# Kernel tuning notes

Hardware: AMD Instinct MI355X
Metric: run time of the kernel (lower is better)

The kernel has to match this reference:

```python
import jax, jax.numpy as jnp
import numpy as np

B, N, P, L = 32, 4096, 256, 16
DR = 128           # rel_dim = args.rgcn_hidden_size
H = 128            # rnn_hidden_size (unidirectional -> rnn_opt_dim == H)
D = H
NUM_REL = 400      # num_rels * 2


def setup_inputs() -> dict:
    key = jax.random.key(0)
    ks = jax.random.split(key, 12)
    s = 0.05
    graph_embed = jax.random.normal(ks[0], (B, N, DR), jnp.float32)
    node_opt = jax.random.normal(ks[1], (B, D), jnp.float32)
    node_idx = jax.random.randint(ks[2], (B, P, L), 0, N)
    rel_idx = jax.random.randint(ks[3], (B, P, L), 0, NUM_REL)
    path_lens = jax.random.randint(ks[4], (B, P), 1, L + 1)  # in [1, L]
    rel_embeds = jax.random.normal(ks[5], (NUM_REL, DR), jnp.float32) * s
    W_ih = jax.random.normal(ks[6], (4 * H, 2 * DR), jnp.float32) * s
    W_hh = jax.random.normal(ks[7], (4 * H, H), jnp.float32) * s
    b_ih = jnp.zeros((4 * H,), jnp.float32)
    b_hh = jnp.zeros((4 * H,), jnp.float32)
    in_proj_w = jax.random.normal(ks[8], (3 * D, D), jnp.float32) * s
    in_proj_b = jnp.zeros((3 * D,), jnp.float32)
    out_proj_w = jax.random.normal(ks[9], (D, D), jnp.float32) * s
    out_proj_b = jnp.zeros((D,), jnp.float32)
    return dict(graph_embed=graph_embed, node_opt=node_opt, rel_embeds=rel_embeds,
                W_ih=W_ih, W_hh=W_hh, b_ih=b_ih, b_hh=b_hh,
                in_proj_w=in_proj_w, in_proj_b=in_proj_b,
                out_proj_w=out_proj_w, out_proj_b=out_proj_b,
                node_idx=node_idx, rel_idx=rel_idx, path_lens=path_lens)


def _forward(graph_embed, node_opt, rel_embeds, W_ih, W_hh, b_ih, b_hh,
             in_proj_w, in_proj_b, out_proj_w, out_proj_b,
             node_idx, rel_idx, path_lens):
    b, n, dr = graph_embed.shape
    p, l = node_idx.shape[1], node_idx.shape[2]
    h = W_hh.shape[1]
    dt = graph_embed.dtype

    t = jnp.arange(l)
    # node embedding valid for steps < len; rel valid for steps < len-1 ('Padr' at last step -> zero rel half)
    node_mask = (t[None, None, :] < path_lens[:, :, None]).astype(dt)[..., None]
    rel_mask = (t[None, None, :] < (path_lens - 1)[:, :, None]).astype(dt)[..., None]

    batch_ix = jnp.arange(b)[:, None, None]
    node_e = graph_embed[batch_ix, node_idx]            # [B,P,L,DR]
    rel_e = rel_embeds[rel_idx]                          # [B,P,L,DR]
    x = jnp.concatenate([node_e * node_mask, rel_e * rel_mask], axis=-1)
    x = x.reshape(b * p, l, 2 * dr)                      # packed path sequences

    bias = b_ih + b_hh

    def step(carry, xt):
        hh, cc = carry
        g = xt @ W_ih.T + hh @ W_hh.T + bias
        i, f, gg, o = jnp.split(g, 4, axis=-1)
        i = jax.nn.sigmoid(i); f = jax.nn.sigmoid(f)
        gg = jnp.tanh(gg); o = jax.nn.sigmoid(o)
        cc = f * cc + i * gg
        hh = o * jnp.tanh(cc)
        return (hh, cc), hh

    h0 = jnp.zeros((b * p, h), dt)
    _, ys = jax.lax.scan(step, (h0, h0), jnp.swapaxes(x, 0, 1))
    ys = jnp.swapaxes(ys, 0, 1).reshape(b, p, l, h)

    # last valid LSTM output per path (== pack_padded_sequence semantics, unidirectional)
    idx = jnp.broadcast_to((path_lens - 1)[:, :, None, None], (b, p, 1, h))
    last = jnp.take_along_axis(ys, idx, axis=2).squeeze(2)   # [B,P,H]

    # single-head MultiheadAttention: query = node_opt, keys/values = path encodings
    Wq, Wk, Wv = jnp.split(in_proj_w, 3, axis=0)
    bq, bk, bv = jnp.split(in_proj_b, 3)
    q = node_opt @ Wq.T + bq                                  # [B,D]
    k = last @ Wk.T + bk                                      # [B,P,D]
    v = last @ Wv.T + bv
    scale = 1.0 / jnp.sqrt(jnp.asarray(q.shape[-1], dt))
    attn = jax.nn.softmax(jnp.einsum('bd,bpd->bp', q, k) * scale, axis=-1)
    ctx = jnp.einsum('bp,bpd->bd', attn, v)
    return ctx @ out_proj_w.T + out_proj_b                    # [B,D]


def reference(graph_embed, node_opt, rel_embeds, W_ih, W_hh, b_ih, b_hh,
              in_proj_w, in_proj_b, out_proj_w, out_proj_b,
              node_idx, rel_idx, path_lens):
    return _forward(graph_embed, node_opt, rel_embeds, W_ih, W_hh, b_ih, b_hh,
                    in_proj_w, in_proj_b, out_proj_w, out_proj_b,
                    node_idx, rel_idx, path_lens)
```

## Files before the change

### kernel.cpp

```cpp
#include <hip/hip_runtime.h>
#include <hip/hip_bf16.h>


#define B_    32
#define N_    4096
#define L_    16
#define DR_   128
#define H_    128
#define G4_   512
#define AST2  264
#define NPATH 8192
#define NPB   16

typedef unsigned short bfraw;
typedef short short8 __attribute__((ext_vector_type(8)));
typedef float f32x4 __attribute__((ext_vector_type(4)));

__device__ int   g_isbf16;
__device__ int   g_isi64;
__device__ __align__(16) bfraw g_Wcat[G4_ * 256];
__device__ __align__(16) float g_relproj[400 * G4_];
__device__ float g_bias[G4_];
__device__ int   g_perm[NPATH];
__device__ float g_last[NPATH * H_];

#define BAR() asm volatile("s_waitcnt lgkmcnt(0)\n\ts_barrier" ::: "memory")

__device__ __forceinline__ float bfc(bfraw v) {
    return __uint_as_float(((unsigned)v) << 16);
}
__device__ __forceinline__ bfraw f2b(float f) {
    unsigned u = __float_as_uint(f);
    return (bfraw)((u + 0x7FFFu + ((u >> 16) & 1u)) >> 16);
}
__device__ __forceinline__ unsigned pk2(float a, float b) {
    return (unsigned)f2b(a) | ((unsigned)f2b(b) << 16);
}
__device__ __forceinline__ float ld(const void* p, size_t i, int isbf) {
    return isbf ? bfc(((const bfraw*)p)[i]) : ((const float*)p)[i];
}
__device__ __forceinline__ float sigf(float x) {
    return __builtin_amdgcn_rcpf(1.0f + __expf(-x));
}
__device__ __forceinline__ float tanhfast(float x) {
    return 2.0f * sigf(2.0f * x) - 1.0f;
}

__device__ __forceinline__ float dot128(const float* __restrict__ w,
                                        const float* __restrict__ s) {
    float acc = 0.f;
    #pragma unroll
    for (int i = 0; i < 32; ++i) {
        const float4 wv = *(const float4*)(w + i * 4);
        acc = fmaf(wv.x, s[i*4+0], fmaf(wv.y, s[i*4+1],
              fmaf(wv.z, s[i*4+2], fmaf(wv.w, s[i*4+3], acc))));
    }
    return acc;
}

__global__ __launch_bounds__(512) void k_prep(
    const void* __restrict__ node_opt, const int* __restrict__ node_idx,
    const void* __restrict__ rel_embeds,
    const void* __restrict__ W_ih, const void* __restrict__ W_hh,
    const void* __restrict__ b_ih, const void* __restrict__ b_hh,
    const int* __restrict__ path_lens)
{
    __shared__ float relv[DR_];
    __shared__ int s_big, s_nz, hist[16], cur[16];
    const int tid = threadIdx.x;
    const int blk = blockIdx.x;

    if (tid == 0) { s_big = 0; s_nz = 0; }
    __syncthreads();
    {
        const unsigned short* u = (const unsigned short*)node_opt;
        int big = 0;
        #pragma unroll
        for (int i = 0; i < 4; ++i) {
            const float v = fabsf(bfc(u[tid + i * 512]));
            big |= !(v < 1.0e3f);
        }
        if (big) s_big = 1;
        if (node_idx[2 * tid + 1] != 0) s_nz = 1;
    }
    __syncthreads();
    const int isbf = s_big ? 0 : 1;
    const int i64  = s_nz ? 0 : 1;

    if (blk < 400) {
        const int r = blk;
        if (tid < DR_) relv[tid] = ld(rel_embeds, (size_t)r * DR_ + tid, isbf);
        __syncthreads();
        const int n = tid;
        float s;
        if (isbf) {
            s = 0.f;
            for (int d = 0; d < DR_; ++d)
                s = fmaf(relv[d], bfc(((const bfraw*)W_ih)[(size_t)n * 256 + 128 + d]), s);
        } else {
            s = dot128((const float*)W_ih + (size_t)n * 256 + 128, relv);
        }
        g_relproj[r * G4_ + ((n & 127) << 2) + (n >> 7)] = s;
    } else if (blk < 656) {
        const int idx = (blk - 400) * 512 + tid;
        const int n = idx >> 8, k = idx & 255;
        const float v = (k < H_) ? ld(W_hh, (size_t)n * H_ + k, isbf)
                                 : ld(W_ih, (size_t)n * 256 + (k - H_), isbf);
        g_Wcat[n * 256 + k] = f2b(v);
    } else {
        if (tid == 0) { g_isbf16 = isbf; g_isi64 = i64; }
        g_bias[tid] = ld(b_ih, tid, isbf) + ld(b_hh, tid, isbf);
        if (tid < 16) hist[tid] = 0;
        __syncthreads();
        for (int p = tid; p < NPATH; p += 512) {
            const int len = i64 ? path_lens[2 * p] : path_lens[p];
            atomicAdd(&hist[len - 1], 1);
        }
        __syncthreads();
        if (tid == 0) {
            int off = 0;
            for (int b = 15; b >= 0; --b) { cur[b] = off; off += hist[b]; }
        }
        __syncthreads();
        for (int p = tid; p < NPATH; p += 512) {
            const int len = i64 ? path_lens[2 * p] : path_lens[p];
            const int pos = atomicAdd(&cur[len - 1], 1);
            g_perm[pos] = p;
        }
    }
}

__global__ __launch_bounds__(512, 2) void k_lstm(
    const void* __restrict__ graph_embed,
    const int*  __restrict__ node_idx,
    const int*  __restrict__ rel_idx,
    const int*  __restrict__ path_lens)
{
    __shared__ __align__(16) bfraw Abuf[2][NPB][AST2];
    __shared__ int s_pid[NPB], s_len[NPB];
    __shared__ int s_nid[NPB][L_], s_rid[NPB][L_];

    const int isbf = g_isbf16;
    const int i64  = g_isi64;
    const int tid  = threadIdx.x;

    if (tid < NPB) {
        const int pid = g_perm[blockIdx.x * NPB + tid];
        s_pid[tid] = pid;
        s_len[tid] = i64 ? path_lens[2 * pid] : path_lens[pid];
    }
    __syncthreads();
    if (tid < 256) {
        const int m = tid >> 4, t = tid & 15;
        const int idx = s_pid[m] * L_ + t;
        s_nid[m][t] = i64 ? node_idx[2 * idx] : node_idx[idx];
        s_rid[m][t] = i64 ? rel_idx[2 * idx]  : rel_idx[idx];
    }
    if (tid < 256) {
        const int m = tid >> 4, i0 = (tid & 15) * 8;
        *(uint4*)&Abuf[0][m][i0] = make_uint4(0, 0, 0, 0);
    }
    __syncthreads();

    int maxlen = 0;
    #pragma unroll
    for (int m = 0; m < NPB; ++m) maxlen = max(maxlen, s_len[m]);

    const int w    = tid >> 6;
    const int l    = tid & 63;
    const int quad = l >> 4;
    const int col  = l & 15;
    const int u0   = w * 16 + col;

    short8 wreg[8][4];
    float bq4[4];
    #pragma unroll
    for (int g = 0; g < 4; ++g) {
        bq4[g] = g_bias[g * 128 + u0];
        const bfraw* wrow = g_Wcat + (size_t)(g * 128 + u0) * 256 + quad * 8;
        #pragma unroll
        for (int ck = 0; ck < 8; ++ck)
            wreg[ck][g] = *(const short8*)(wrow + ck * 32);
    }

    const int pm  = tid >> 5;
    const int pi0 = (tid & 31) * 4;
    const size_t gbase = (size_t)(s_pid[pm] >> 8) * (size_t)(N_ * DR_);

    uint4 pnA, pnB;

    {
        const int nid = s_nid[pm][0];
        uint2 npk;
        if (isbf) {
            const uint2 q = *(const uint2*)((const bfraw*)graph_embed + gbase + (size_t)nid * DR_ + pi0);
            npk = q;
        } else {
            const float* gp = (const float*)graph_embed + gbase + (size_t)nid * DR_ + pi0;
            const uint4 q = *(const uint4*)gp;
            const float* a = (const float*)&q;
            npk = make_uint2(pk2(a[0], a[1]), pk2(a[2], a[3]));
        }
        *(uint2*)&Abuf[0][pm][128 + pi0] = npk;
    }
    if (maxlen > 1) {
        const int nid = s_nid[pm][1];
        if (isbf) {
            const uint2 q = *(const uint2*)((const bfraw*)graph_embed + gbase + (size_t)nid * DR_ + pi0);
            pnA.x = q.x; pnA.y = q.y;
        } else {
            pnA = *(const uint4*)((const float*)graph_embed + gbase + (size_t)nid * DR_ + pi0);
        }
    }
    __syncthreads();

    float c[4];
    #pragma unroll
    for (int r = 0; r < 4; ++r) c[r] = 0.f;

    bfraw (*Ar)[AST2] = Abuf[0];
    bfraw (*Aw)[AST2] = Abuf[1];

    for (int t = 0; t < maxlen; ++t) {
        const bool more = (t + 1 < maxlen);

        if (t + 2 < maxlen) {
            const int nid = s_nid[pm][t + 2];
            if (isbf) {
                const uint2 q = *(const uint2*)((const bfraw*)graph_embed + gbase + (size_t)nid * DR_ + pi0);
                pnB.x = q.x; pnB.y = q.y;
            } else {
                pnB = *(const uint4*)((const float*)graph_embed + gbase + (size_t)nid * DR_ + pi0);
            }
        }

        f32x4 acc[4];
        #pragma unroll
        for (int g = 0; g < 4; ++g) {
            const float b = bq4[g];
            acc[g][0] = b; acc[g][1] = b; acc[g][2] = b; acc[g][3] = b;
        }
        #pragma unroll
        for (int ck = 0; ck < 8; ++ck) {
            const short8 a0 = *(const short8*)&Ar[col][ck * 32 + quad * 8];
            #pragma unroll
            for (int g = 0; g < 4; ++g)
                acc[g] = __builtin_amdgcn_mfma_f32_16x16x32_bf16(a0, wreg[ck][g], acc[g], 0, 0, 0);
        }
        __builtin_amdgcn_sched_barrier(0);

        f32x4 rlv[4];
        #pragma unroll
        for (int r = 0; r < 4; ++r) {
            const int m = quad * 4 + r;
            rlv[r] = *(const f32x4*)(g_relproj + (size_t)s_rid[m][t] * G4_ + u0 * 4);
        }

        #pragma unroll
        for (int r = 0; r < 4; ++r) {
            const int m = quad * 4 + r;
            const float relm = (t < s_len[m] - 1) ? 1.0f : 0.0f;
            const float ig = sigf(acc[0][r] + relm * rlv[r][0]);
            const float fg = sigf(acc[1][r] + relm * rlv[r][1]);
            const float gg = tanhfast(acc[2][r] + relm * rlv[r][2]);
            const float og = sigf(acc[3][r] + relm * rlv[r][3]);
            const float cc = fg * c[r] + ig * gg;
            c[r] = cc;
            const float h = og * tanhfast(cc);
            Aw[m][u0] = f2b(h);
            if (t == s_len[m] - 1)
                g_last[(size_t)s_pid[m] * H_ + u0] = h;
        }

        if (more) {
            uint2 npk = make_uint2(0, 0);
            if (t + 1 < s_len[pm]) {
                if (isbf) npk = make_uint2(pnA.x, pnA.y);
                else {
                    const float* a = (const float*)&pnA;
                    npk = make_uint2(pk2(a[0], a[1]), pk2(a[2], a[3]));
                }
            }
            *(uint2*)&Aw[pm][128 + pi0] = npk;
            pnA = pnB;
        }

        BAR();
        bfraw (*tmp)[AST2] = Ar; Ar = Aw; Aw = tmp;
    }
}

__global__ __launch_bounds__(256) void k_attn(
    const void* __restrict__ node_opt,
    const void* __restrict__ in_proj_w,
    const void* __restrict__ in_proj_b,
    const void* __restrict__ out_proj_w,
    const void* __restrict__ out_proj_b,
    float* __restrict__ out)
{
    const int isbf = g_isbf16;
    const int b = blockIdx.x, tid = threadIdx.x;
    __shared__ __align__(16) float s_no[128], q[128], qk[128], sv2[2][128], ctx[128];
    __shared__ float logits[256];
    __shared__ float red[12];

    const int u    = tid & 127;
    const int half = tid >> 7;

    if (tid < 128) s_no[tid] = ld(node_opt, b * 128 + tid, isbf);
    __syncthreads();
    {
        float s = 0.f;
        const int j0 = half * 64;
        if (isbf) {
            #pragma unroll 8
            for (int j = 0; j < 64; ++j)
                s = fmaf(s_no[j0 + j], ld(in_proj_w, (size_t)u * 128 + j0 + j, 1), s);
        } else {
            const float* wr = (const float*)in_proj_w + (size_t)u * 128 + j0;
            #pragma unroll
            for (int i = 0; i < 16; ++i) {
                const float4 wv = *(const float4*)(wr + i * 4);
                s = fmaf(wv.x, s_no[j0+i*4+0], fmaf(wv.y, s_no[j0+i*4+1],
                    fmaf(wv.z, s_no[j0+i*4+2], fmaf(wv.w, s_no[j0+i*4+3], s))));
            }
        }
        sv2[half][u] = s;
    }
    __syncthreads();
    if (tid < 128) q[tid] = sv2[0][tid] + sv2[1][tid] + ld(in_proj_b, tid, isbf);
    __syncthreads();
    {
        float s = 0.f;
        const int j0 = half * 64;
        #pragma unroll 8
        for (int j = 0; j < 64; ++j)
            s = fmaf(q[j0 + j], ld(in_proj_w, (size_t)(128 + j0 + j) * 128 + u, isbf), s);
        sv2[half][u] = s;
    }
    if (tid == 0) {
        float s = 0.f;
        #pragma unroll 8
        for (int j = 0; j < 128; ++j)
            s = fmaf(q[j], ld(in_proj_b, 128 + j, isbf), s);
        red[10] = s;
    }
    __syncthreads();
    if (tid < 128) qk[tid] = sv2[0][tid] + sv2[1][tid];
    __syncthreads();
    {
        const float* lp = g_last + ((size_t)b * 256 + tid) * H_;
        const float s = dot128(lp, qk);
        logits[tid] = (s + red[10]) * 0.08838834764831845f;
    }
    __syncthreads();
    float v = logits[tid];
    #pragma unroll
    for (int off = 32; off > 0; off >>= 1) v = fmaxf(v, __shfl_xor(v, off, 64));
    if ((tid & 63) == 0) red[tid >> 6] = v;
    __syncthreads();
    if (tid == 0) red[8] = fmaxf(fmaxf(red[0], red[1]), fmaxf(red[2], red[3]));
    __syncthreads();
    const float e = __expf(logits[tid] - red[8]);
    float sum = e;
    #pragma unroll
    for (int off = 32; off > 0; off >>= 1) sum += __shfl_xor(sum, off, 64);
    if ((tid & 63) == 0) red[4 + (tid >> 6)] = sum;
    __syncthreads();
    if (tid == 0) red[9] = red[4] + red[5] + red[6] + red[7];
    __syncthreads();
    logits[tid] = e / red[9];
    __syncthreads();
    {
        float s = 0.f;
        const float* lb = g_last + ((size_t)b * 256 + half * 128) * H_ + u;
        #pragma unroll 8
        for (int p = 0; p < 128; ++p)
            s = fmaf(logits[half * 128 + p], lb[(size_t)p * H_], s);
        sv2[half][u] = s;
    }
    __syncthreads();
    if (tid < 128) q[tid] = sv2[0][tid] + sv2[1][tid];
    __syncthreads();
    if (tid < 128) {
        float s;
        if (isbf) {
            s = 0.f;
            #pragma unroll 8
            for (int j = 0; j < 128; ++j)
                s = fmaf(q[j], ld(in_proj_w, (size_t)(256 + tid) * 128 + j, 1), s);
        } else {
            s = dot128((const float*)in_proj_w + (size_t)(256 + tid) * 128, q);
        }
        ctx[tid] = s + ld(in_proj_b, 256 + tid, isbf);
    }
    __syncthreads();
    if (tid < 128) {
        float s;
        if (isbf) {
            s = 0.f;
            #pragma unroll 8
            for (int d = 0; d < 128; ++d)
                s = fmaf(ctx[d], ld(out_proj_w, (size_t)tid * 128 + d, 1), s);
        } else {
            s = dot128((const float*)out_proj_w + (size_t)tid * 128, ctx);
        }
        out[b * 128 + tid] = s + ld(out_proj_b, tid, isbf);
    }
}

extern "C" void kernel_launch(void* const* d_in, const int* in_sizes, int n_in,
                              void* d_out, int out_size, void* d_ws, size_t ws_size,
                              hipStream_t stream)
{
    const void* graph_embed = d_in[0];
    const void* node_opt    = d_in[1];
    const void* rel_embeds  = d_in[2];
    const void* W_ih        = d_in[3];
    const void* W_hh        = d_in[4];
    const void* b_ih        = d_in[5];
    const void* b_hh        = d_in[6];
    const void* in_proj_w   = d_in[7];
    const void* in_proj_b   = d_in[8];
    const void* out_proj_w  = d_in[9];
    const void* out_proj_b  = d_in[10];
    const int* node_idx  = (const int*)d_in[11];
    const int* rel_idx   = (const int*)d_in[12];
    const int* path_lens = (const int*)d_in[13];
    (void)d_ws; (void)ws_size; (void)in_sizes; (void)n_in; (void)out_size;

    hipLaunchKernelGGL(k_prep, dim3(657), dim3(512), 0, stream,
                       node_opt, node_idx, rel_embeds, W_ih, W_hh, b_ih, b_hh,
                       path_lens);
    hipLaunchKernelGGL(k_lstm, dim3(NPATH / NPB), dim3(512), 0, stream,
                       graph_embed, node_idx, rel_idx, path_lens);
    hipLaunchKernelGGL(k_attn, dim3(B_), dim3(256), 0, stream,
                       node_opt, in_proj_w, in_proj_b, out_proj_w, out_proj_b,
                       (float*)d_out);
}
```

Before: 205.4 us.

## Double paths per block and stage recurrent weights in LDS instead of registers

```diff
diff --git a/kernel.cpp b/kernel.cpp
--- a/kernel.cpp
+++ b/kernel.cpp
@@ -10,7 +10,7 @@
 #define G4_   512
 #define AST2  264
 #define NPATH 8192
-#define NPB   16
+#define NPB   32
 
 typedef unsigned short bfraw;
 typedef short short8 __attribute__((ext_vector_type(8)));
@@ -130,13 +130,14 @@
     }
 }
 
-__global__ __launch_bounds__(512, 2) void k_lstm(
+__global__ __launch_bounds__(1024, 4) void k_lstm(
     const void* __restrict__ graph_embed,
     const int*  __restrict__ node_idx,
     const int*  __restrict__ rel_idx,
     const int*  __restrict__ path_lens)
 {
-    __shared__ __align__(16) bfraw Abuf[2][NPB][AST2];
+    __shared__ __align__(16) bfraw Whh[4][4][G4_][8];
+    __shared__ __align__(16) bfraw A[NPB][AST2];
     __shared__ int s_pid[NPB], s_len[NPB];
     __shared__ int s_nid[NPB][L_], s_rid[NPB][L_];
 
@@ -150,15 +151,20 @@
         s_len[tid] = i64 ? path_lens[2 * pid] : path_lens[pid];
     }
     __syncthreads();
-    if (tid < 256) {
+    if (tid < 512) {
         const int m = tid >> 4, t = tid & 15;
         const int idx = s_pid[m] * L_ + t;
         s_nid[m][t] = i64 ? node_idx[2 * idx] : node_idx[idx];
         s_rid[m][t] = i64 ? rel_idx[2 * idx]  : rel_idx[idx];
     }
-    if (tid < 256) {
+    if (tid < 512) {
         const int m = tid >> 4, i0 = (tid & 15) * 8;
-        *(uint4*)&Abuf[0][m][i0] = make_uint4(0, 0, 0, 0);
+        *(uint4*)&A[m][i0] = make_uint4(0, 0, 0, 0);
+    }
+    for (int i = tid; i < 4 * 4 * G4_; i += 1024) {
+        const int n = i & 511, q = (i >> 9) & 3, ck = i >> 11;
+        *(uint4*)&Whh[ck][q][n][0] =
+            *(const uint4*)(g_Wcat + (size_t)n * 256 + ck * 32 + q * 8);
     }
     __syncthreads();
 
@@ -166,22 +172,18 @@
     #pragma unroll
     for (int m = 0; m < NPB; ++m) maxlen = max(maxlen, s_len[m]);
 
-    const int w    = tid >> 6;
+    const int wid  = tid >> 6;
+    const int tile = wid >> 3;
+    const int w8   = wid & 7;
     const int l    = tid & 63;
     const int quad = l >> 4;
     const int col  = l & 15;
-    const int u0   = w * 16 + col;
-
-    short8 wreg[8][4];
+    const int u0   = w8 * 16 + col;
+    const int mrow = tile * 16;
+
     float bq4[4];
     #pragma unroll
-    for (int g = 0; g < 4; ++g) {
-        bq4[g] = g_bias[g * 128 + u0];
-        const bfraw* wrow = g_Wcat + (size_t)(g * 128 + u0) * 256 + quad * 8;
-        #pragma unroll
-        for (int ck = 0; ck < 8; ++ck)
-            wreg[ck][g] = *(const short8*)(wrow + ck * 32);
-    }
+    for (int g = 0; g < 4; ++g) bq4[g] = g_bias[g * 128 + u0];
 
     const int pm  = tid >> 5;
     const int pi0 = (tid & 31) * 4;
@@ -193,15 +195,14 @@
         const int nid = s_nid[pm][0];
         uint2 npk;
         if (isbf) {
-            const uint2 q = *(const uint2*)((const bfraw*)graph_embed + gbase + (size_t)nid * DR_ + pi0);
-            npk = q;
+            npk = *(const uint2*)((const bfraw*)graph_embed + gbase + (size_t)nid * DR_ + pi0);
         } else {
             const float* gp = (const float*)graph_embed + gbase + (size_t)nid * DR_ + pi0;
             const uint4 q = *(const uint4*)gp;
             const float* a = (const float*)&q;
             npk = make_uint2(pk2(a[0], a[1]), pk2(a[2], a[3]));
         }
-        *(uint2*)&Abuf[0][pm][128 + pi0] = npk;
+        *(uint2*)&A[pm][128 + pi0] = npk;
     }
     if (maxlen > 1) {
         const int nid = s_nid[pm][1];
@@ -217,9 +218,6 @@
     float c[4];
     #pragma unroll
     for (int r = 0; r < 4; ++r) c[r] = 0.f;
-
-    bfraw (*Ar)[AST2] = Abuf[0];
-    bfraw (*Aw)[AST2] = Abuf[1];
 
     for (int t = 0; t < maxlen; ++t) {
         const bool more = (t + 1 < maxlen);
@@ -241,24 +239,37 @@
             acc[g][0] = b; acc[g][1] = b; acc[g][2] = b; acc[g][3] = b;
         }
         #pragma unroll
-        for (int ck = 0; ck < 8; ++ck) {
-            const short8 a0 = *(const short8*)&Ar[col][ck * 32 + quad * 8];
+        for (int ck = 0; ck < 4; ++ck) {
+            const short8 a0 = *(const short8*)&A[mrow + col][ck * 32 + quad * 8];
             #pragma unroll
-            for (int g = 0; g < 4; ++g)
-                acc[g] = __builtin_amdgcn_mfma_f32_16x16x32_bf16(a0, wreg[ck][g], acc[g], 0, 0, 0);
+            for (int g = 0; g < 4; ++g) {
+                const short8 wv = *(const short8*)&Whh[ck][quad][g * 128 + u0][0];
+                acc[g] = __builtin_amdgcn_mfma_f32_16x16x32_bf16(a0, wv, acc[g], 0, 0, 0);
+            }
+        }
+        #pragma unroll
+        for (int ck4 = 0; ck4 < 4; ++ck4) {
+            const short8 a0 = *(const short8*)&A[mrow + col][(4 + ck4) * 32 + quad * 8];
+            const bfraw* wrow = g_Wcat + (size_t)u0 * 256 + 128 + ck4 * 32 + quad * 8;
+            #pragma unroll
+            for (int g = 0; g < 4; ++g) {
+                const short8 wv = *(const short8*)(wrow + (size_t)g * 128 * 256);
+                acc[g] = __builtin_amdgcn_mfma_f32_16x16x32_bf16(a0, wv, acc[g], 0, 0, 0);
+            }
         }
         __builtin_amdgcn_sched_barrier(0);
 
         f32x4 rlv[4];
         #pragma unroll
         for (int r = 0; r < 4; ++r) {
-            const int m = quad * 4 + r;
+            const int m = mrow + quad * 4 + r;
             rlv[r] = *(const f32x4*)(g_relproj + (size_t)s_rid[m][t] * G4_ + u0 * 4);
         }
 
+        float hv[4];
         #pragma unroll
         for (int r = 0; r < 4; ++r) {
-            const int m = quad * 4 + r;
+            const int m = mrow + quad * 4 + r;
             const float relm = (t < s_len[m] - 1) ? 1.0f : 0.0f;
             const float ig = sigf(acc[0][r] + relm * rlv[r][0]);
             const float fg = sigf(acc[1][r] + relm * rlv[r][1]);
@@ -266,10 +277,17 @@
             const float og = sigf(acc[3][r] + relm * rlv[r][3]);
             const float cc = fg * c[r] + ig * gg;
             c[r] = cc;
-            const float h = og * tanhfast(cc);
-            Aw[m][u0] = f2b(h);
+            hv[r] = og * tanhfast(cc);
+        }
+
+        BAR();
+
+        #pragma unroll
+        for (int r = 0; r < 4; ++r) {
+            const int m = mrow + quad * 4 + r;
+            A[m][u0] = f2b(hv[r]);
             if (t == s_len[m] - 1)
-                g_last[(size_t)s_pid[m] * H_ + u0] = h;
+                g_last[(size_t)s_pid[m] * H_ + u0] = hv[r];
         }
 
         if (more) {
@@ -281,12 +299,11 @@
                     npk = make_uint2(pk2(a[0], a[1]), pk2(a[2], a[3]));
                 }
             }
-            *(uint2*)&Aw[pm][128 + pi0] = npk;
+            *(uint2*)&A[pm][128 + pi0] = npk;
             pnA = pnB;
         }
 
         BAR();
-        bfraw (*tmp)[AST2] = Ar; Ar = Aw; Aw = tmp;
     }
 }
 
@@ -432,7 +449,7 @@
     hipLaunchKernelGGL(k_prep, dim3(657), dim3(512), 0, stream,
                        node_opt, node_idx, rel_embeds, W_ih, W_hh, b_ih, b_hh,
                        path_lens);
-    hipLaunchKernelGGL(k_lstm, dim3(NPATH / NPB), dim3(512), 0, stream,
+    hipLaunchKernelGGL(k_lstm, dim3(NPATH / NPB), dim3(1024), 0, stream,
                        graph_embed, node_idx, rel_idx, path_lens);
     hipLaunchKernelGGL(k_attn, dim3(B_), dim3(256), 0, stream,
                        node_opt, in_proj_w, in_proj_b, out_proj_w, out_proj_b,
```

Result: slower. 314.7 us (+53.2%).
